# Optimization experiments

Hardware: AMD Instinct MI355X
Metric: run time of the kernel (lower is better)

## Reference

```python
import jax, jax.numpy as jnp
import numpy as np

B, D, W = 65536, 256, 1024

def setup_inputs() -> dict:
    key = jax.random.key(0)
    k1, k2, k3, k4 = jax.random.split(key, 4)
    z = jax.random.normal(k1, (B, D), dtype=jnp.float32)
    # PyTorch Linear init: U(-1/sqrt(fan_in), 1/sqrt(fan_in))
    s1 = 1.0 / np.sqrt(D)
    s2 = 1.0 / np.sqrt(W)
    W1 = jax.random.uniform(k2, (W, D), dtype=jnp.float32, minval=-s1, maxval=s1)
    b1 = jax.random.uniform(k3, (W,), dtype=jnp.float32, minval=-s1, maxval=s1)
    W2 = jax.random.uniform(k4, (D, W), dtype=jnp.float32, minval=-s2, maxval=s2)
    t = jnp.zeros((1,), dtype=jnp.float32)
    return {"t": t, "z": z, "W1": W1, "b1": b1, "W2": W2}

def reference(t, z, W1, b1, W2):
    # dynamics: f(z) = W2 @ softplus(W1 z + b1)   (t is unused; autonomous ODE)
    pre = z @ W1.T + b1                 # [B, W]
    h = jax.nn.softplus(pre)            # [B, W]
    dz_dt = h @ W2.T                    # [B, D]
    # trace of Jacobian, analytic:
    # df_i/dz_i = sum_j W2[i,j] * sigmoid(pre_j) * W1[j,i]
    # => trace_b = sigmoid(pre_b) . M, with M_j = sum_i W1[j,i] * W2[i,j]
    M = jnp.einsum('ji,ij->j', W1, W2)  # [W]
    trace = jax.nn.sigmoid(pre) @ M     # [B]
    dlogpz_dt = -trace[:, None]         # [B, 1]
    return (dz_dt, dlogpz_dt)
```

## Files before the change

### kernel.cpp

```cpp
#include <hip/hip_runtime.h>
#include <cstdint>
#include <cstddef>

#define B_N 65536
#define D_N 256
#define W_N 1024

typedef __bf16 bf16x8 __attribute__((ext_vector_type(8)));
typedef float f32x4 __attribute__((ext_vector_type(4)));
typedef unsigned short u16x8 __attribute__((ext_vector_type(8)));

__device__ __forceinline__ unsigned short f2bf(float f) {
  unsigned u = __float_as_uint(f);
  u += 0x7fffu + ((u >> 16) & 1u);
  return (unsigned short)(u >> 16);
}

__device__ __forceinline__ void lds_barrier() {
  __builtin_amdgcn_sched_barrier(0);
  asm volatile("s_waitcnt lgkmcnt(0)" ::: "memory");
  __builtin_amdgcn_s_barrier();
  __builtin_amdgcn_sched_barrier(0);
}

__global__ __launch_bounds__(256) void prep_kernel(
    const float* __restrict__ W1, const float* __restrict__ W2,
    unsigned short* __restrict__ W1b, unsigned short* __restrict__ W2b,
    float* __restrict__ M) {
  const int j = blockIdx.x;
  const int t = threadIdx.x;
  const int gid = j * 256 + t;
  float w1 = W1[gid];
  float w2g = W2[gid];
  W1b[gid] = f2bf(w1);
  W2b[gid] = f2bf(w2g);
  float p = w1 * W2[t * W_N + j];
  #pragma unroll
  for (int m = 32; m; m >>= 1) p += __shfl_xor(p, m);
  __shared__ float red[4];
  if ((t & 63) == 0) red[t >> 6] = p;
  __syncthreads();
  if (t == 0) M[j] = red[0] + red[1] + red[2] + red[3];
}

__global__ __launch_bounds__(256, 2) void flow_kernel(
    const float* __restrict__ z, const float* __restrict__ b1,
    const unsigned short* __restrict__ W1b, const unsigned short* __restrict__ W2b,
    const float* __restrict__ M, float* __restrict__ dz, float* __restrict__ tr) {
  __shared__ __align__(16) unsigned short z_sh[64 * 256];
  __shared__ __align__(16) unsigned short h_sh[64 * 256];

  const int tid = threadIdx.x;
  const int wave = tid >> 6;
  const int lane = tid & 63;
  const int l15 = lane & 15;
  const int q = lane >> 4;
  const int row0 = blockIdx.x * 64;

  #pragma unroll
  for (int it = 0; it < 8; ++it) {
    int id = it * 256 + tid;
    int m = id >> 5;
    int o = id & 31;
    const float* gp = z + (size_t)(row0 + m) * D_N + o * 8;
    f32x4 a = *(const f32x4*)gp;
    f32x4 b = *(const f32x4*)(gp + 4);
    u16x8 v;
    v[0] = f2bf(a[0]); v[1] = f2bf(a[1]); v[2] = f2bf(a[2]); v[3] = f2bf(a[3]);
    v[4] = f2bf(b[0]); v[5] = f2bf(b[1]); v[6] = f2bf(b[2]); v[7] = f2bf(b[3]);
    int slot = (((o >> 2) * 4 + (m >> 4)) * 64 + (o & 3) * 16 + (m & 15));
    *(u16x8*)(z_sh + slot * 8) = v;
  }
  __syncthreads();

  f32x4 acc2[4][4];
  #pragma unroll
  for (int a = 0; a < 4; ++a)
    #pragma unroll
    for (int b = 0; b < 4; ++b)
      acc2[a][b] = (f32x4){0.f, 0.f, 0.f, 0.f};
  float trp[4][4];
  #pragma unroll
  for (int a = 0; a < 4; ++a)
    #pragma unroll
    for (int r = 0; r < 4; ++r) trp[a][r] = 0.f;

  #pragma unroll 1
  for (int c = 0; c < 4; ++c) {
    const int j0 = c * 256;

    const unsigned short* w1p[4];
    #pragma unroll
    for (int tn = 0; tn < 4; ++tn)
      w1p[tn] = W1b + (size_t)(j0 + wave * 64 + tn * 16 + l15) * D_N + q * 8;

    bf16x8 bq[3][4];
    #pragma unroll
    for (int p = 0; p < 3; ++p)
      #pragma unroll
      for (int tn = 0; tn < 4; ++tn)
        bq[p][tn] = *(const bf16x8*)(w1p[tn] + p * 32);

    float b1c[4], Mc[4];
    #pragma unroll
    for (int tn = 0; tn < 4; ++tn) {
      int jg = j0 + wave * 64 + tn * 16 + l15;
      b1c[tn] = b1[jg];
      Mc[tn] = M[jg];
    }

    f32x4 acc1[4][4];
    #pragma unroll
    for (int a = 0; a < 4; ++a)
      #pragma unroll
      for (int b = 0; b < 4; ++b)
        acc1[a][b] = (f32x4){0.f, 0.f, 0.f, 0.f};

    #pragma unroll
    for (int ks = 0; ks < 8; ++ks) {
      bf16x8 afr[4];
      #pragma unroll
      for (int tm = 0; tm < 4; ++tm)
        afr[tm] = *(const bf16x8*)(z_sh + ((ks * 4 + tm) * 64 + lane) * 8);
      #pragma unroll
      for (int tm = 0; tm < 4; ++tm)
        #pragma unroll
        for (int tn = 0; tn < 4; ++tn)
          acc1[tm][tn] = __builtin_amdgcn_mfma_f32_16x16x32_bf16(
              afr[tm], bq[ks % 3][tn], acc1[tm][tn], 0, 0, 0);
      if (ks < 5) {
        #pragma unroll
        for (int tn = 0; tn < 4; ++tn)
          bq[ks % 3][tn] = *(const bf16x8*)(w1p[tn] + (ks + 3) * 32);
      }
    }

    const unsigned short* w2p[4];
    #pragma unroll
    for (int tn = 0; tn < 4; ++tn)
      w2p[tn] = W2b + (size_t)(wave * 64 + tn * 16 + l15) * W_N + j0 + q * 8;
    bf16x8 cq[3][4];
    #pragma unroll
    for (int p = 0; p < 3; ++p)
      #pragma unroll
      for (int tn = 0; tn < 4; ++tn)
        cq[p][tn] = *(const bf16x8*)(w2p[tn] + p * 32);

    lds_barrier();

    #pragma unroll
    for (int tn = 0; tn < 4; ++tn) {
      const int jl = wave * 64 + tn * 16 + l15;
      const float b1v = b1c[tn];
      const float Mv = Mc[tn];
      const int slot_base = ((jl >> 5) * 4) * 64 + ((jl >> 3) & 3) * 16;
      const int byte_lo = (jl & 7);
      #pragma unroll
      for (int tm = 0; tm < 4; ++tm) {
        #pragma unroll
        for (int r = 0; r < 4; ++r) {
          float x = acc1[tm][tn][r] + b1v;
          float e = __expf(-fabsf(x));
          float inv = __builtin_amdgcn_rcpf(1.0f + e);
          float sig = (x >= 0.f) ? inv : (1.0f - inv);
          float sp = fmaxf(x, 0.f) + __logf(1.0f + e);
          trp[tm][r] += sig * Mv;
          int slot = slot_base + tm * 64 + (q * 4 + r);
          h_sh[slot * 8 + byte_lo] = f2bf(sp);
        }
      }
    }

    lds_barrier();

    #pragma unroll
    for (int ks = 0; ks < 8; ++ks) {
      bf16x8 afr[4];
      #pragma unroll
      for (int tm = 0; tm < 4; ++tm)
        afr[tm] = *(const bf16x8*)(h_sh + ((ks * 4 + tm) * 64 + lane) * 8);
      #pragma unroll
      for (int tm = 0; tm < 4; ++tm)
        #pragma unroll
        for (int tn = 0; tn < 4; ++tn)
          acc2[tm][tn] = __builtin_amdgcn_mfma_f32_16x16x32_bf16(
              afr[tm], cq[ks % 3][tn], acc2[tm][tn], 0, 0, 0);
      if (ks < 5) {
        #pragma unroll
        for (int tn = 0; tn < 4; ++tn)
          cq[ks % 3][tn] = *(const bf16x8*)(w2p[tn] + (ks + 3) * 32);
      }
    }
  }

  #pragma unroll
  for (int tm = 0; tm < 4; ++tm)
    #pragma unroll
    for (int tn = 0; tn < 4; ++tn)
      #pragma unroll
      for (int r = 0; r < 4; ++r)
        dz[(size_t)(row0 + tm * 16 + q * 4 + r) * D_N + wave * 64 + tn * 16 + l15] =
            acc2[tm][tn][r];

  #pragma unroll
  for (int tm = 0; tm < 4; ++tm) {
    #pragma unroll
    for (int r = 0; r < 4; ++r) {
      float v = trp[tm][r];
      v += __shfl_xor(v, 1);
      v += __shfl_xor(v, 2);
      v += __shfl_xor(v, 4);
      v += __shfl_xor(v, 8);
      if (l15 == 0) atomicAdd(tr + row0 + tm * 16 + q * 4 + r, -v);
    }
  }
}

extern "C" void kernel_launch(void* const* d_in, const int* in_sizes, int n_in,
                              void* d_out, int out_size, void* d_ws, size_t ws_size,
                              hipStream_t stream) {
  (void)in_sizes; (void)n_in; (void)out_size; (void)ws_size;
  const float* z  = (const float*)d_in[1];
  const float* W1 = (const float*)d_in[2];
  const float* b1 = (const float*)d_in[3];
  const float* W2 = (const float*)d_in[4];
  float* dz = (float*)d_out;
  float* tr = dz + (size_t)B_N * D_N;

  unsigned short* W1b = (unsigned short*)d_ws;
  unsigned short* W2b = W1b + (size_t)W_N * D_N;
  float* M = (float*)(W2b + (size_t)W_N * D_N);

  hipMemsetAsync(tr, 0, B_N * sizeof(float), stream);
  prep_kernel<<<dim3(W_N), dim3(256), 0, stream>>>(W1, W2, W1b, W2b, M);
  flow_kernel<<<dim3(B_N / 64), dim3(256), 0, stream>>>(z, b1, W1b, W2b, M, dz, tr);
}
```

Before: 255.3 us.

## Split fused MLP kernel into two kernels with bf16 hidden activations in workspace

Replaces the single fused kernel with two passes when the workspace is large enough. The first computes the hidden layer, softplus and the trace and writes bf16 hidden activations to global memory in an MFMA-friendly layout. The second runs the second GEMM over them. This frees the h_sh LDS buffer and registers to allow 3 blocks per CU and drops the in-loop barriers. The cost is roughly 128 MB of extra global write and read traffic, plus scattered 2-byte stores. Whether the new path runs depends on the workspace size.

```diff
diff --git a/kernel.cpp b/kernel.cpp
--- a/kernel.cpp
+++ b/kernel.cpp
@@ -14,13 +14,6 @@
   unsigned u = __float_as_uint(f);
   u += 0x7fffu + ((u >> 16) & 1u);
   return (unsigned short)(u >> 16);
-}
-
-__device__ __forceinline__ void lds_barrier() {
-  __builtin_amdgcn_sched_barrier(0);
-  asm volatile("s_waitcnt lgkmcnt(0)" ::: "memory");
-  __builtin_amdgcn_s_barrier();
-  __builtin_amdgcn_sched_barrier(0);
 }
 
 __global__ __launch_bounds__(256) void prep_kernel(
@@ -43,12 +36,11 @@
   if (t == 0) M[j] = red[0] + red[1] + red[2] + red[3];
 }
 
-__global__ __launch_bounds__(256, 2) void flow_kernel(
+__global__ __launch_bounds__(256, 3) void flow_a(
     const float* __restrict__ z, const float* __restrict__ b1,
-    const unsigned short* __restrict__ W1b, const unsigned short* __restrict__ W2b,
-    const float* __restrict__ M, float* __restrict__ dz, float* __restrict__ tr) {
+    const unsigned short* __restrict__ W1b, const float* __restrict__ M,
+    unsigned short* __restrict__ Hb, float* __restrict__ tr) {
   __shared__ __align__(16) unsigned short z_sh[64 * 256];
-  __shared__ __align__(16) unsigned short h_sh[64 * 256];
 
   const int tid = threadIdx.x;
   const int wave = tid >> 6;
@@ -56,6 +48,7 @@
   const int l15 = lane & 15;
   const int q = lane >> 4;
   const int row0 = blockIdx.x * 64;
+  const size_t hbase = (size_t)blockIdx.x * (64 * W_N);
 
   #pragma unroll
   for (int it = 0; it < 8; ++it) {
@@ -73,12 +66,6 @@
   }
   __syncthreads();
 
-  f32x4 acc2[4][4];
-  #pragma unroll
-  for (int a = 0; a < 4; ++a)
-    #pragma unroll
-    for (int b = 0; b < 4; ++b)
-      acc2[a][b] = (f32x4){0.f, 0.f, 0.f, 0.f};
   float trp[4][4];
   #pragma unroll
   for (int a = 0; a < 4; ++a)
@@ -89,17 +76,12 @@
   for (int c = 0; c < 4; ++c) {
     const int j0 = c * 256;
 
-    const unsigned short* w1p[4];
-    #pragma unroll
-    for (int tn = 0; tn < 4; ++tn)
-      w1p[tn] = W1b + (size_t)(j0 + wave * 64 + tn * 16 + l15) * D_N + q * 8;
-
-    bf16x8 bq[3][4];
-    #pragma unroll
-    for (int p = 0; p < 3; ++p)
-      #pragma unroll
-      for (int tn = 0; tn < 4; ++tn)
-        bq[p][tn] = *(const bf16x8*)(w1p[tn] + p * 32);
+    f32x4 acc1[4][4];
+    #pragma unroll
+    for (int a = 0; a < 4; ++a)
+      #pragma unroll
+      for (int b = 0; b < 4; ++b)
+        acc1[a][b] = (f32x4){0.f, 0.f, 0.f, 0.f};
 
     float b1c[4], Mc[4];
     #pragma unroll
@@ -109,98 +91,49 @@
       Mc[tn] = M[jg];
     }
 
-    f32x4 acc1[4][4];
-    #pragma unroll
-    for (int a = 0; a < 4; ++a)
-      #pragma unroll
-      for (int b = 0; b < 4; ++b)
-        acc1[a][b] = (f32x4){0.f, 0.f, 0.f, 0.f};
-
     #pragma unroll
     for (int ks = 0; ks < 8; ++ks) {
       bf16x8 afr[4];
       #pragma unroll
       for (int tm = 0; tm < 4; ++tm)
         afr[tm] = *(const bf16x8*)(z_sh + ((ks * 4 + tm) * 64 + lane) * 8);
+      bf16x8 bfr[4];
+      #pragma unroll
+      for (int tn = 0; tn < 4; ++tn)
+        bfr[tn] = *(const bf16x8*)(W1b +
+            (size_t)(j0 + wave * 64 + tn * 16 + l15) * D_N + ks * 32 + q * 8);
       #pragma unroll
       for (int tm = 0; tm < 4; ++tm)
         #pragma unroll
         for (int tn = 0; tn < 4; ++tn)
           acc1[tm][tn] = __builtin_amdgcn_mfma_f32_16x16x32_bf16(
-              afr[tm], bq[ks % 3][tn], acc1[tm][tn], 0, 0, 0);
-      if (ks < 5) {
-        #pragma unroll
-        for (int tn = 0; tn < 4; ++tn)
-          bq[ks % 3][tn] = *(const bf16x8*)(w1p[tn] + (ks + 3) * 32);
-      }
-    }
-
-    const unsigned short* w2p[4];
-    #pragma unroll
-    for (int tn = 0; tn < 4; ++tn)
-      w2p[tn] = W2b + (size_t)(wave * 64 + tn * 16 + l15) * W_N + j0 + q * 8;
-    bf16x8 cq[3][4];
-    #pragma unroll
-    for (int p = 0; p < 3; ++p)
-      #pragma unroll
-      for (int tn = 0; tn < 4; ++tn)
-        cq[p][tn] = *(const bf16x8*)(w2p[tn] + p * 32);
-
-    lds_barrier();
+              afr[tm], bfr[tn], acc1[tm][tn], 0, 0, 0);
+    }
 
     #pragma unroll
     for (int tn = 0; tn < 4; ++tn) {
-      const int jl = wave * 64 + tn * 16 + l15;
       const float b1v = b1c[tn];
       const float Mv = Mc[tn];
-      const int slot_base = ((jl >> 5) * 4) * 64 + ((jl >> 3) & 3) * 16;
-      const int byte_lo = (jl & 7);
+      const int ksg = c * 8 + wave * 2 + (tn >> 1);
+      const int colp = ((tn & 1) * 2 + (l15 >> 3)) * 16;
+      const int e = l15 & 7;
       #pragma unroll
       for (int tm = 0; tm < 4; ++tm) {
         #pragma unroll
         for (int r = 0; r < 4; ++r) {
           float x = acc1[tm][tn][r] + b1v;
-          float e = __expf(-fabsf(x));
-          float inv = __builtin_amdgcn_rcpf(1.0f + e);
+          float ex = __expf(-fabsf(x));
+          float inv = __builtin_amdgcn_rcpf(1.0f + ex);
           float sig = (x >= 0.f) ? inv : (1.0f - inv);
-          float sp = fmaxf(x, 0.f) + __logf(1.0f + e);
+          float sp = fmaxf(x, 0.f) + __logf(1.0f + ex);
           trp[tm][r] += sig * Mv;
-          int slot = slot_base + tm * 64 + (q * 4 + r);
-          h_sh[slot * 8 + byte_lo] = f2bf(sp);
+          size_t idx = hbase +
+              (size_t)(((ksg * 4 + tm) * 64 + colp + q * 4 + r)) * 8 + e;
+          Hb[idx] = f2bf(sp);
         }
       }
     }
-
-    lds_barrier();
-
-    #pragma unroll
-    for (int ks = 0; ks < 8; ++ks) {
-      bf16x8 afr[4];
-      #pragma unroll
-      for (int tm = 0; tm < 4; ++tm)
-        afr[tm] = *(const bf16x8*)(h_sh + ((ks * 4 + tm) * 64 + lane) * 8);
-      #pragma unroll
-      for (int tm = 0; tm < 4; ++tm)
-        #pragma unroll
-        for (int tn = 0; tn < 4; ++tn)
-          acc2[tm][tn] = __builtin_amdgcn_mfma_f32_16x16x32_bf16(
-              afr[tm], cq[ks % 3][tn], acc2[tm][tn], 0, 0, 0);
-      if (ks < 5) {
-        #pragma unroll
-        for (int tn = 0; tn < 4; ++tn)
-          cq[ks % 3][tn] = *(const bf16x8*)(w2p[tn] + (ks + 3) * 32);
-      }
-    }
-  }
-
-  #pragma unroll
-  for (int tm = 0; tm < 4; ++tm)
-    #pragma unroll
-    for (int tn = 0; tn < 4; ++tn)
-      #pragma unroll
-      for (int r = 0; r < 4; ++r)
-        dz[(size_t)(row0 + tm * 16 + q * 4 + r) * D_N + wave * 64 + tn * 16 + l15] =
-            acc2[tm][tn][r];
+  }
 
   #pragma unroll
   for (int tm = 0; tm < 4; ++tm) {
@@ -216,10 +149,236 @@
   }
 }
 
+__global__ __launch_bounds__(256, 3) void flow_b(
+    const unsigned short* __restrict__ Hb, const unsigned short* __restrict__ W2b,
+    float* __restrict__ dz) {
+  const int tid = threadIdx.x;
+  const int wave = tid >> 6;
+  const int lane = tid & 63;
+  const int l15 = lane & 15;
+  const int q = lane >> 4;
+  const int row0 = blockIdx.x * 64;
+  const unsigned short* hb = Hb + (size_t)blockIdx.x * (64 * W_N);
+
+  f32x4 acc2[4][4];
+  #pragma unroll
+  for (int a = 0; a < 4; ++a)
+    #pragma unroll
+    for (int b = 0; b < 4; ++b)
+      acc2[a][b] = (f32x4){0.f, 0.f, 0.f, 0.f};
+
+  #pragma unroll 4
+  for (int ks = 0; ks < 32; ++ks) {
+    bf16x8 afr[4];
+    #pragma unroll
+    for (int tm = 0; tm < 4; ++tm)
+      afr[tm] = *(const bf16x8*)(hb + ((ks * 4 + tm) * 64 + lane) * 8);
+    bf16x8 bfr[4];
+    #pragma unroll
+    for (int tn = 0; tn < 4; ++tn)
+      bfr[tn] = *(const bf16x8*)(W2b +
+          (size_t)(wave * 64 + tn * 16 + l15) * W_N + ks * 32 + q * 8);
+    #pragma unroll
+    for (int tm = 0; tm < 4; ++tm)
+      #pragma unroll
+      for (int tn = 0; tn < 4; ++tn)
+        acc2[tm][tn] = __builtin_amdgcn_mfma_f32_16x16x32_bf16(
+            afr[tm], bfr[tn], acc2[tm][tn], 0, 0, 0);
+  }
+
+  #pragma unroll
+  for (int tm = 0; tm < 4; ++tm)
+    #pragma unroll
+    for (int tn = 0; tn < 4; ++tn)
+      #pragma unroll
+      for (int r = 0; r < 4; ++r)
+        dz[(size_t)(row0 + tm * 16 + q * 4 + r) * D_N + wave * 64 + tn * 16 + l15] =
+            acc2[tm][tn][r];
+}
+
+__device__ __forceinline__ void lds_barrier() {
+  __builtin_amdgcn_sched_barrier(0);
+  asm volatile("s_waitcnt lgkmcnt(0)" ::: "memory");
+  __builtin_amdgcn_s_barrier();
+  __builtin_amdgcn_sched_barrier(0);
+}
+
+__global__ __launch_bounds__(256, 2) void flow_kernel(
+    const float* __restrict__ z, const float* __restrict__ b1,
+    const unsigned short* __restrict__ W1b, const unsigned short* __restrict__ W2b,
+    const float* __restrict__ M, float* __restrict__ dz, float* __restrict__ tr) {
+  __shared__ __align__(16) unsigned short z_sh[64 * 256];
+  __shared__ __align__(16) unsigned short h_sh[64 * 256];
+
+  const int tid = threadIdx.x;
+  const int wave = tid >> 6;
+  const int lane = tid & 63;
+  const int l15 = lane & 15;
+  const int q = lane >> 4;
+  const int row0 = blockIdx.x * 64;
+
+  #pragma unroll
+  for (int it = 0; it < 8; ++it) {
+    int id = it * 256 + tid;
+    int m = id >> 5;
+    int o = id & 31;
+    const float* gp = z + (size_t)(row0 + m) * D_N + o * 8;
+    f32x4 a = *(const f32x4*)gp;
+    f32x4 b = *(const f32x4*)(gp + 4);
+    u16x8 v;
+    v[0] = f2bf(a[0]); v[1] = f2bf(a[1]); v[2] = f2bf(a[2]); v[3] = f2bf(a[3]);
+    v[4] = f2bf(b[0]); v[5] = f2bf(b[1]); v[6] = f2bf(b[2]); v[7] = f2bf(b[3]);
+    int slot = (((o >> 2) * 4 + (m >> 4)) * 64 + (o & 3) * 16 + (m & 15));
+    *(u16x8*)(z_sh + slot * 8) = v;
+  }
+  __syncthreads();
+
+  f32x4 acc2[4][4];
+  #pragma unroll
+  for (int a = 0; a < 4; ++a)
+    #pragma unroll
+    for (int b = 0; b < 4; ++b)
+      acc2[a][b] = (f32x4){0.f, 0.f, 0.f, 0.f};
+  float trp[4][4];
+  #pragma unroll
+  for (int a = 0; a < 4; ++a)
+    #pragma unroll
+    for (int r = 0; r < 4; ++r) trp[a][r] = 0.f;
+
+  #pragma unroll 1
+  for (int c = 0; c < 4; ++c) {
+    const int j0 = c * 256;
+    const unsigned short* w1p[4];
+    #pragma unroll
+    for (int tn = 0; tn < 4; ++tn)
+      w1p[tn] = W1b + (size_t)(j0 + wave * 64 + tn * 16 + l15) * D_N + q * 8;
+
+    bf16x8 bq[3][4];
+    #pragma unroll
+    for (int p = 0; p < 3; ++p)
+      #pragma unroll
+      for (int tn = 0; tn < 4; ++tn)
+        bq[p][tn] = *(const bf16x8*)(w1p[tn] + p * 32);
+
+    float b1c[4], Mc[4];
+    #pragma unroll
+    for (int tn = 0; tn < 4; ++tn) {
+      int jg = j0 + wave * 64 + tn * 16 + l15;
+      b1c[tn] = b1[jg];
+      Mc[tn] = M[jg];
+    }
+
+    f32x4 acc1[4][4];
+    #pragma unroll
+    for (int a = 0; a < 4; ++a)
+      #pragma unroll
+      for (int b = 0; b < 4; ++b)
+        acc1[a][b] = (f32x4){0.f, 0.f, 0.f, 0.f};
+
+    #pragma unroll
+    for (int ks = 0; ks < 8; ++ks) {
+      bf16x8 afr[4];
+      #pragma unroll
+      for (int tm = 0; tm < 4; ++tm)
+        afr[tm] = *(const bf16x8*)(z_sh + ((ks * 4 + tm) * 64 + lane) * 8);
+      #pragma unroll
+      for (int tm = 0; tm < 4; ++tm)
+        #pragma unroll
+        for (int tn = 0; tn < 4; ++tn)
+          acc1[tm][tn] = __builtin_amdgcn_mfma_f32_16x16x32_bf16(
+              afr[tm], bq[ks % 3][tn], acc1[tm][tn], 0, 0, 0);
+      if (ks < 5) {
+        #pragma unroll
+        for (int tn = 0; tn < 4; ++tn)
+          bq[ks % 3][tn] = *(const bf16x8*)(w1p[tn] + (ks + 3) * 32);
+      }
+    }
+
+    const unsigned short* w2p[4];
+    #pragma unroll
+    for (int tn = 0; tn < 4; ++tn)
+      w2p[tn] = W2b + (size_t)(wave * 64 + tn * 16 + l15) * W_N + j0 + q * 8;
+    bf16x8 cq[3][4];
+    #pragma unroll
+    for (int p = 0; p < 3; ++p)
+      #pragma unroll
+      for (int tn = 0; tn < 4; ++tn)
+        cq[p][tn] = *(const bf16x8*)(w2p[tn] + p * 32);
+
+    lds_barrier();
+
+    #pragma unroll
+    for (int tn = 0; tn < 4; ++tn) {
+      const int jl = wave * 64 + tn * 16 + l15;
+      const float b1v = b1c[tn];
+      const float Mv = Mc[tn];
+      const int slot_base = ((jl >> 5) * 4) * 64 + ((jl >> 3) & 3) * 16;
+      const int byte_lo = (jl & 7);
+      #pragma unroll
+      for (int tm = 0; tm < 4; ++tm) {
+        #pragma unroll
+        for (int r = 0; r < 4; ++r) {
+          float x = acc1[tm][tn][r] + b1v;
+          float ex = __expf(-fabsf(x));
+          float inv = __builtin_amdgcn_rcpf(1.0f + ex);
+          float sig = (x >= 0.f) ? inv : (1.0f - inv);
+          float sp = fmaxf(x, 0.f) + __logf(1.0f + ex);
+          trp[tm][r] += sig * Mv;
+          int slot = slot_base + tm * 64 + (q * 4 + r);
+          h_sh[slot * 8 + byte_lo] = f2bf(sp);
+        }
+      }
+    }
+
+    lds_barrier();
+
+    #pragma unroll
+    for (int ks = 0; ks < 8; ++ks) {
+      bf16x8 afr[4];
+      #pragma unroll
+      for (int tm = 0; tm < 4; ++tm)
+        afr[tm] = *(const bf16x8*)(h_sh + ((ks * 4 + tm) * 64 + lane) * 8);
+      #pragma unroll
+      for (int tm = 0; tm < 4; ++tm)
+        #pragma unroll
+        for (int tn = 0; tn < 4; ++tn)
+          acc2[tm][tn] = __builtin_amdgcn_mfma_f32_16x16x32_bf16(
+              afr[tm], cq[ks % 3][tn], acc2[tm][tn], 0, 0, 0);
+      if (ks < 5) {
+        #pragma unroll
+        for (int tn = 0; tn < 4; ++tn)
+          cq[ks % 3][tn] = *(const bf16x8*)(w2p[tn] + (ks + 3) * 32);
+      }
+    }
+  }
+
+  #pragma unroll
+  for (int tm = 0; tm < 4; ++tm)
+    #pragma unroll
+    for (int tn = 0; tn < 4; ++tn)
+      #pragma unroll
+      for (int r = 0; r < 4; ++r)
+        dz[(size_t)(row0 + tm * 16 + q * 4 + r) * D_N + wave * 64 + tn * 16 + l15] =
+            acc2[tm][tn][r];
+
+  #pragma unroll
+  for (int tm = 0; tm < 4; ++tm) {
+    #pragma unroll
+    for (int r = 0; r < 4; ++r) {
+      float v = trp[tm][r];
+      v += __shfl_xor(v, 1);
+      v += __shfl_xor(v, 2);
+      v += __shfl_xor(v, 4);
+      v += __shfl_xor(v, 8);
+      if (l15 == 0) atomicAdd(tr + row0 + tm * 16 + q * 4 + r, -v);
+    }
+  }
+}
+
 extern "C" void kernel_launch(void* const* d_in, const int* in_sizes, int n_in,
                               void* d_out, int out_size, void* d_ws, size_t ws_size,
                               hipStream_t stream) {
-  (void)in_sizes; (void)n_in; (void)out_size; (void)ws_size;
+  (void)in_sizes; (void)n_in; (void)out_size;
   const float* z  = (const float*)d_in[1];
   const float* W1 = (const float*)d_in[2];
   const float* b1 = (const float*)d_in[3];
@@ -230,8 +389,17 @@
   unsigned short* W1b = (unsigned short*)d_ws;
   unsigned short* W2b = W1b + (size_t)W_N * D_N;
   float* M = (float*)(W2b + (size_t)W_N * D_N);
+  unsigned short* Hb = (unsigned short*)(M + W_N);
+
+  const size_t need = (size_t)2 * W_N * D_N * 2 + (size_t)W_N * 4 +
+                      (size_t)B_N * W_N * 2;
 
   hipMemsetAsync(tr, 0, B_N * sizeof(float), stream);
   prep_kernel<<<dim3(W_N), dim3(256), 0, stream>>>(W1, W2, W1b, W2b, M);
-  flow_kernel<<<dim3(B_N / 64), dim3(256), 0, stream>>>(z, b1, W1b, W2b, M, dz, tr);
-}
+  if (ws_size >= need) {
+    flow_a<<<dim3(B_N / 64), dim3(256), 0, stream>>>(z, b1, W1b, M, Hb, tr);
+    flow_b<<<dim3(B_N / 64), dim3(256), 0, stream>>>(Hb, W2b, dz);
+  } else {
+    flow_kernel<<<dim3(B_N / 64), dim3(256), 0, stream>>>(z, b1, W1b, W2b, M, dz, tr);
+  }
+}
```

Result: slower. 449.5 us (+76.1%).
